# Optimization experiments

Measured on AMD Instinct MI355X. Metric: run time of the kernel, lower is better.

Reference implementation:

```python
import jax, jax.numpy as jnp
import numpy as np

HIDDEN = 1024
HEADS = 16
HEAD = HIDDEN // HEADS


def setup_inputs() -> dict:
    key = jax.random.key(0)
    ks = jax.random.split(key, 10)
    s = 1.0 / np.sqrt(HIDDEN)
    inp = {
        "x": jax.random.normal(ks[0], (2, 2048, HIDDEN), dtype=jnp.float32),
        "Wq": jax.random.uniform(ks[1], (HIDDEN, HIDDEN), jnp.float32, -s, s),
        "bq": jnp.zeros((HIDDEN,), jnp.float32),
        "Wk": jax.random.uniform(ks[2], (HIDDEN, HIDDEN), jnp.float32, -s, s),
        "bk": jnp.zeros((HIDDEN,), jnp.float32),
        "Wv": jax.random.uniform(ks[3], (HIDDEN, HIDDEN), jnp.float32, -s, s),
        "bv": jnp.zeros((HIDDEN,), jnp.float32),
        "Wo": jax.random.uniform(ks[4], (HIDDEN, HIDDEN), jnp.float32, -s, s),
        "bo": jnp.zeros((HIDDEN,), jnp.float32),
        "ln_g": jnp.ones((HIDDEN,), jnp.float32),
        "ln_b": jnp.zeros((HIDDEN,), jnp.float32),
    }
    return inp


def reference(x, Wq, bq, Wk, bk, Wv, bv, Wo, bo, ln_g, ln_b):
    B, S, H = x.shape
    # pre-LN (eps=1e-5 like torch LayerNorm)
    mu = jnp.mean(x, axis=-1, keepdims=True)
    var = jnp.mean(jnp.square(x - mu), axis=-1, keepdims=True)
    xn = (x - mu) * jax.lax.rsqrt(var + 1e-5) * ln_g + ln_b
    # QKV projections (torch Linear: x @ W.T + b) -> [B,S,heads,head]
    q = (xn @ Wq.T + bq).reshape(B, S, HEADS, HEAD)
    k = (xn @ Wk.T + bk).reshape(B, S, HEADS, HEAD)
    v = (xn @ Wv.T + bv).reshape(B, S, HEADS, HEAD)
    # scaled dot-product attention, naive full scores [B,heads,S,S]
    scores = jnp.einsum("bqhd,bkhd->bhqk", q, k) / jnp.sqrt(jnp.float32(HEAD))
    attn = jax.nn.softmax(scores, axis=-1)
    ctx = jnp.einsum("bhqk,bkhd->bqhd", attn, v).reshape(B, S, H)
    out = ctx @ Wo.T + bo
    return x + out  # dropout is identity in eval
```

## Files before the change

kernel.cpp:

```cpp
#include <hip/hip_runtime.h>
#include <hip/hip_bf16.h>
#include <stdint.h>

#define HID 1024
#define SEQ 2048
#define BATCH 2
#define NHEADS 16
#define HEADDIM 64
#define MROWS (BATCH*SEQ)

#define GAS __attribute__((address_space(1)))
#define LAS __attribute__((address_space(3)))

typedef __attribute__((ext_vector_type(8))) __bf16 bf16x8;
typedef __attribute__((ext_vector_type(4))) float f32x4;
typedef __attribute__((ext_vector_type(16))) float f32x16;

__device__ __forceinline__ ushort f2bf(float f) {
  union { float f; uint32_t u; } v; v.f = f;
  return (ushort)((v.u + 0x7FFFu + ((v.u >> 16) & 1u)) >> 16);
}

__device__ __forceinline__ void gl_lds16(const void* g, void* l) {
  __builtin_amdgcn_global_load_lds((const GAS void*)g, (LAS void*)l, 16, 0, 0);
}

__device__ __forceinline__ uint32_t cvtpk(float a, float b) {
  uint32_t r;
  asm("v_cvt_pk_bf16_f32 %0, %1, %2" : "=v"(r) : "v"(a), "v"(b));
  return r;
}

__device__ __forceinline__ void pl32swap(uint32_t& a, uint32_t& b) {
  asm("v_permlane32_swap_b32 %0, %1" : "+v"(a), "+v"(b));
}

__global__ __launch_bounds__(256) void k_cvt(const float* __restrict__ Wq,
                                             const float* __restrict__ Wk,
                                             const float* __restrict__ Wv,
                                             const float* __restrict__ Wo,
                                             ushort* __restrict__ dst) {
  int mat = blockIdx.y;
  const float* src = (mat == 0) ? Wq : (mat == 1) ? Wk : (mat == 2) ? Wv : Wo;
  int off = (blockIdx.x * 256 + threadIdx.x) * 4;
  float4 v = *(const float4*)(src + off);
  ushort4 o;
  o.x = f2bf(v.x); o.y = f2bf(v.y); o.z = f2bf(v.z); o.w = f2bf(v.w);
  *(ushort4*)(dst + (size_t)mat * (HID * HID) + off) = o;
}

__global__ __launch_bounds__(256) void k_ln(const float* __restrict__ x,
                                            const float* __restrict__ g,
                                            const float* __restrict__ b,
                                            ushort* __restrict__ xn) {
  int row = blockIdx.x;
  int t = threadIdx.x;
  const float* xr = x + (size_t)row * HID;
  float4 v = *(const float4*)(xr + t * 4);
  float s = v.x + v.y + v.z + v.w;
  float s2 = v.x * v.x + v.y * v.y + v.z * v.z + v.w * v.w;
  for (int m = 1; m < 64; m <<= 1) { s += __shfl_xor(s, m); s2 += __shfl_xor(s2, m); }
  __shared__ float ws[4], ws2[4];
  int wid = t >> 6;
  if ((t & 63) == 0) { ws[wid] = s; ws2[wid] = s2; }
  __syncthreads();
  s = ws[0] + ws[1] + ws[2] + ws[3];
  s2 = ws2[0] + ws2[1] + ws2[2] + ws2[3];
  float mu = s * (1.0f / HID);
  float var = s2 * (1.0f / HID) - mu * mu;
  float rstd = rsqrtf(var + 1e-5f);
  float4 gg = *(const float4*)(g + t * 4);
  float4 bb = *(const float4*)(b + t * 4);
  ushort4 o;
  o.x = f2bf((v.x - mu) * rstd * gg.x + bb.x);
  o.y = f2bf((v.y - mu) * rstd * gg.y + bb.y);
  o.z = f2bf((v.z - mu) * rstd * gg.z + bb.z);
  o.w = f2bf((v.w - mu) * rstd * gg.w + bb.w);
  *(ushort4*)(xn + (size_t)row * HID + t * 4) = o;
}

__global__ __launch_bounds__(256) void k_qkv(const ushort* __restrict__ xn,
                                             const ushort* __restrict__ wmat,
                                             const float* __restrict__ bq,
                                             const float* __restrict__ bk,
                                             const float* __restrict__ bv,
                                             ushort* __restrict__ qo,
                                             ushort* __restrict__ ko,
                                             ushort* __restrict__ vo) {
  __shared__ ushort As[128 * 32];
  __shared__ ushort Bs[128 * 32];
  int tid = threadIdx.x;
  int lane = tid & 63;
  int wv = tid >> 6;
  int quad = lane >> 4;
  int l16 = lane & 15;
  int m0 = blockIdx.x * 128;
  int ng = blockIdx.y * 128;
  int mat = ng >> 10;
  int nloc = ng & 1023;
  const ushort* wptr = wmat + (size_t)mat * (HID * HID) + (size_t)nloc * HID;
  const float* bias = (mat == 0) ? bq : (mat == 1) ? bk : bv;
  ushort* outp = (mat == 0) ? qo : (mat == 1) ? ko : vo;
  const float scl = (mat == 0) ? 0.18033688011112042f : 1.0f;

  int arow = tid >> 2;
  int acol = (tid & 3) * 8;
  int wm = (wv >> 1) * 64, wn = (wv & 1) * 64;

  f32x4 acc[4][4] = {};
  for (int k0 = 0; k0 < HID; k0 += 32) {
    __syncthreads();
    for (int t = 0; t < 2; t++) {
      gl_lds16(xn + (size_t)(m0 + t * 64 + arow) * HID + k0 + acol,
               As + t * 2048 + wv * 512);
      gl_lds16(wptr + (size_t)(t * 64 + arow) * HID + k0 + acol,
               Bs + t * 2048 + wv * 512);
    }
    __syncthreads();
    bf16x8 af[4], bfr[4];
    for (int i = 0; i < 4; i++)
      af[i] = *(const bf16x8*)&As[(wm + i * 16 + l16) * 32 + quad * 8];
    for (int n = 0; n < 4; n++)
      bfr[n] = *(const bf16x8*)&Bs[(wn + n * 16 + l16) * 32 + quad * 8];
    for (int i = 0; i < 4; i++)
      for (int n = 0; n < 4; n++)
        acc[i][n] = __builtin_amdgcn_mfma_f32_16x16x32_bf16(af[i], bfr[n], acc[i][n], 0, 0, 0);
  }
  float bv4[4];
  for (int n = 0; n < 4; n++) bv4[n] = bias[nloc + wn + n * 16 + l16];
  for (int i = 0; i < 4; i++) {
    int mrow = m0 + wm + i * 16 + quad * 4;
    for (int n = 0; n < 4; n++) {
      int col = nloc + wn + n * 16 + l16;
      int h = col >> 6, d = col & 63;
      for (int r = 0; r < 4; r++) {
        int m = mrow + r;
        int bidx = m >> 11, sidx = m & 2047;
        size_t dst;
        if (mat == 2)
          dst = (((size_t)(bidx * NHEADS + h) * HEADDIM) + d) * SEQ + sidx;
        else
          dst = (((size_t)(bidx * NHEADS + h) * SEQ) + sidx) * HEADDIM + d;
        outp[dst] = f2bf((acc[i][n][r] + bv4[n]) * scl);
      }
    }
  }
}

#define E2(x) __builtin_amdgcn_exp2f(fminf((x), 80.f))

#define SOFTMAX_PF(S0, S1)                                                     \
    union { uint32_t u[4]; bf16x8 v; } pf0, pf1, pf2, pf3;                     \
    {                                                                          \
      uint32_t c0 = cvtpk(E2(S0[0]),  E2(S0[1]));                              \
      uint32_t c1 = cvtpk(E2(S0[2]),  E2(S0[3]));                              \
      uint32_t c2 = cvtpk(E2(S0[4]),  E2(S0[5]));                              \
      uint32_t c3 = cvtpk(E2(S0[6]),  E2(S0[7]));                              \
      uint32_t c4 = cvtpk(E2(S0[8]),  E2(S0[9]));                              \
      uint32_t c5 = cvtpk(E2(S0[10]), E2(S0[11]));                             \
      uint32_t c6 = cvtpk(E2(S0[12]), E2(S0[13]));                             \
      uint32_t c7 = cvtpk(E2(S0[14]), E2(S0[15]));                             \
      pl32swap(c0, c2); pl32swap(c1, c3); pl32swap(c4, c6); pl32swap(c5, c7);  \
      pf0.u[0] = c0; pf0.u[1] = c1; pf0.u[2] = c2; pf0.u[3] = c3;              \
      pf1.u[0] = c4; pf1.u[1] = c5; pf1.u[2] = c6; pf1.u[3] = c7;              \
    }                                                                          \
    {                                                                          \
      uint32_t c0 = cvtpk(E2(S1[0]),  E2(S1[1]));                              \
      uint32_t c1 = cvtpk(E2(S1[2]),  E2(S1[3]));                              \
      uint32_t c2 = cvtpk(E2(S1[4]),  E2(S1[5]));                              \
      uint32_t c3 = cvtpk(E2(S1[6]),  E2(S1[7]));                              \
      uint32_t c4 = cvtpk(E2(S1[8]),  E2(S1[9]));                              \
      uint32_t c5 = cvtpk(E2(S1[10]), E2(S1[11]));                             \
      uint32_t c6 = cvtpk(E2(S1[12]), E2(S1[13]));                             \
      uint32_t c7 = cvtpk(E2(S1[14]), E2(S1[15]));                             \
      pl32swap(c0, c2); pl32swap(c1, c3); pl32swap(c4, c6); pl32swap(c5, c7);  \
      pf2.u[0] = c0; pf2.u[1] = c1; pf2.u[2] = c2; pf2.u[3] = c3;              \
      pf3.u[0] = c4; pf3.u[1] = c5; pf3.u[2] = c6; pf3.u[3] = c7;              \
    }

#define ATTN_BODY(T, SC0, SC1, SP0, SP1, DO_DMA)                               \
  do {                                                                         \
    if (DO_DMA) {                                                              \
      size_t ko = (size_t)((T) + 1) * 64 * HEADDIM;                            \
      size_t vo = (size_t)((T) + 1) * 64;                                      \
      int kn = kc ^ 1;                                                         \
      gl_lds16(kSrcA + ko, &Ksm[kn][ldsA]);                                    \
      gl_lds16(kSrcB + ko, &Ksm[kn][ldsB]);                                    \
      gl_lds16(vSrcA + vo, &Vsm[vn][ldsA]);                                    \
      gl_lds16(vSrcB + vo, &Vsm[vn][ldsB]);                                    \
    }                                                                          \
    SC0 = (f32x16){}; SC1 = (f32x16){};                                        \
    __builtin_amdgcn_s_setprio(1);                                             \
    _Pragma("unroll")                                                          \
    for (int f = 0; f < 4; f++) {                                              \
      int g = 2 * f + hi;                                                      \
      bf16x8 k0 = *(const bf16x8*)&Ksm[kc][l32 * 64 + ((g ^ rsw) * 8)];        \
      bf16x8 k1 = *(const bf16x8*)&Ksm[kc][(32 + l32) * 64 + ((g ^ rsw) * 8)]; \
      SC0 = __builtin_amdgcn_mfma_f32_32x32x16_bf16(k0, qf[f], SC0, 0, 0, 0);  \
      SC1 = __builtin_amdgcn_mfma_f32_32x32x16_bf16(k1, qf[f], SC1, 0, 0, 0);  \
    }                                                                          \
    __builtin_amdgcn_s_setprio(0);                                             \
    bf16x8 vf[8];                                                              \
    _Pragma("unroll")                                                          \
    for (int kf = 0; kf < 4; kf++) {                                           \
      int g = 2 * kf + hi;                                                     \
      vf[2 * kf]     = *(const bf16x8*)&Vsm[vp][l32 * 64 + ((g ^ rsw) * 8)];   \
      vf[2 * kf + 1] = *(const bf16x8*)&Vsm[vp][(32 + l32) * 64 + ((g ^ rsw) * 8)]; \
    }                                                                          \
    SOFTMAX_PF(SP0, SP1)                                                       \
    __builtin_amdgcn_s_setprio(1);                                             \
    _Pragma("unroll")                                                          \
    for (int kf = 0; kf < 4; kf++) {                                           \
      bf16x8 pv = (kf == 0) ? pf0.v : (kf == 1) ? pf1.v : (kf == 2) ? pf2.v : pf3.v; \
      Oa0 = __builtin_amdgcn_mfma_f32_32x32x16_bf16(pv, vf[2 * kf], Oa0, 0, 0, 0);   \
      Oa1 = __builtin_amdgcn_mfma_f32_32x32x16_bf16(pv, vf[2 * kf + 1], Oa1, 0, 0, 0); \
      Os  = __builtin_amdgcn_mfma_f32_32x32x16_bf16(pv, ones, Os, 0, 0, 0);    \
    }                                                                          \
    __builtin_amdgcn_s_setprio(0);                                             \
    __syncthreads();                                                           \
    if (DO_DMA) kc ^= 1;                                                       \
    { int tmp = vp; vp = vc; vc = vn; vn = tmp; }                              \
  } while (0)

__global__ __launch_bounds__(256, 2) void k_attn(const ushort* __restrict__ Q,
                                                 const ushort* __restrict__ K,
                                                 const ushort* __restrict__ Vt,
                                                 ushort* __restrict__ ctx) {
  __shared__ ushort Ksm[2][64 * 64];
  __shared__ ushort Vsm[3][64 * 64];
  int tid = threadIdx.x, lane = tid & 63, wv = tid >> 6;
  int l32 = lane & 31, hi = lane >> 5;
  int bh = blockIdx.x;
  int q0 = blockIdx.y * 128;
  const ushort* Qb = Q + ((size_t)bh * SEQ + q0 + wv * 32 + l32) * HEADDIM;
  const ushort* Kb = K + (size_t)bh * SEQ * HEADDIM;
  const ushort* Vb = Vt + (size_t)bh * HEADDIM * SEQ;

  bf16x8 qf[4];
#pragma unroll
  for (int f = 0; f < 4; f++)
    qf[f] = *(const bf16x8*)(Qb + f * 16 + hi * 8);

  bf16x8 ones;
#pragma unroll
  for (int j = 0; j < 8; j++) ones[j] = (__bf16)1.0f;

  int gsl = lane & 7;
  int rowA = wv * 8 + (lane >> 3);
  int rowB = 32 + wv * 8 + (lane >> 3);
  const ushort* kSrcA = Kb + rowA * HEADDIM + ((gsl ^ (rowA & 7)) * 8);
  const ushort* kSrcB = Kb + rowB * HEADDIM + ((gsl ^ (rowB & 7)) * 8);
  const ushort* vSrcA = Vb + (size_t)rowA * SEQ + ((gsl ^ (rowA & 7)) * 8);
  const ushort* vSrcB = Vb + (size_t)rowB * SEQ + ((gsl ^ (rowB & 7)) * 8);
  int ldsA = wv * 512;
  int ldsB = 2048 + wv * 512;

  f32x16 Oa0 = {}, Oa1 = {}, Os = {};
  f32x16 sA0, sA1, sB0, sB1;
  int rsw = (l32 & 7);

  gl_lds16(kSrcA, &Ksm[0][ldsA]);
  gl_lds16(kSrcB, &Ksm[0][ldsB]);
  gl_lds16(vSrcA, &Vsm[0][ldsA]);
  gl_lds16(vSrcB, &Vsm[0][ldsB]);
  __syncthreads();

  {
    size_t ko = (size_t)64 * HEADDIM;
    size_t vo = (size_t)64;
    gl_lds16(kSrcA + ko, &Ksm[1][ldsA]);
    gl_lds16(kSrcB + ko, &Ksm[1][ldsB]);
    gl_lds16(vSrcA + vo, &Vsm[1][ldsA]);
    gl_lds16(vSrcB + vo, &Vsm[1][ldsB]);
    sA0 = (f32x16){}; sA1 = (f32x16){};
    __builtin_amdgcn_s_setprio(1);
#pragma unroll
    for (int f = 0; f < 4; f++) {
      int g = 2 * f + hi;
      bf16x8 k0 = *(const bf16x8*)&Ksm[0][l32 * 64 + ((g ^ rsw) * 8)];
      bf16x8 k1 = *(const bf16x8*)&Ksm[0][(32 + l32) * 64 + ((g ^ rsw) * 8)];
      sA0 = __builtin_amdgcn_mfma_f32_32x32x16_bf16(k0, qf[f], sA0, 0, 0, 0);
      sA1 = __builtin_amdgcn_mfma_f32_32x32x16_bf16(k1, qf[f], sA1, 0, 0, 0);
    }
    __builtin_amdgcn_s_setprio(0);
    __syncthreads();
  }

  int kc = 1, vp = 0, vc = 1, vn = 2;
  for (int t = 1; t < 31; t += 2) {
    ATTN_BODY(t,     sB0, sB1, sA0, sA1, true);
    ATTN_BODY(t + 1, sA0, sA1, sB0, sB1, true);
  }
  ATTN_BODY(31, sB0, sB1, sA0, sA1, false);

  {
    bf16x8 vf[8];
#pragma unroll
    for (int kf = 0; kf < 4; kf++) {
      int g = 2 * kf + hi;
      vf[2 * kf]     = *(const bf16x8*)&Vsm[vp][l32 * 64 + ((g ^ rsw) * 8)];
      vf[2 * kf + 1] = *(const bf16x8*)&Vsm[vp][(32 + l32) * 64 + ((g ^ rsw) * 8)];
    }
    SOFTMAX_PF(sB0, sB1)
    __builtin_amdgcn_s_setprio(1);
#pragma unroll
    for (int kf = 0; kf < 4; kf++) {
      bf16x8 pv = (kf == 0) ? pf0.v : (kf == 1) ? pf1.v : (kf == 2) ? pf2.v : pf3.v;
      Oa0 = __builtin_amdgcn_mfma_f32_32x32x16_bf16(pv, vf[2 * kf], Oa0, 0, 0, 0);
      Oa1 = __builtin_amdgcn_mfma_f32_32x32x16_bf16(pv, vf[2 * kf + 1], Oa1, 0, 0, 0);
      Os  = __builtin_amdgcn_mfma_f32_32x32x16_bf16(pv, ones, Os, 0, 0, 0);
    }
    __builtin_amdgcn_s_setprio(0);
  }

  int bidx = bh >> 4, h = bh & 15;
#pragma unroll
  for (int r = 0; r < 16; r++) {
    float inv = 1.0f / Os[r];
    int qloc = (r & 3) + 8 * (r >> 2) + 4 * hi;
    int sidx = q0 + wv * 32 + qloc;
    size_t base = ((size_t)(bidx * SEQ) + sidx) * HID + h * HEADDIM;
    ctx[base + l32]      = f2bf(Oa0[r] * inv);
    ctx[base + 32 + l32] = f2bf(Oa1[r] * inv);
  }
}

__global__ __launch_bounds__(256) void k_oproj(const ushort* __restrict__ ctx,
                                               const ushort* __restrict__ wmat,
                                               const float* __restrict__ bo,
                                               const float* __restrict__ x,
                                               float* __restrict__ out) {
  __shared__ ushort As[128 * 32];
  __shared__ ushort Bs[128 * 32];
  int tid = threadIdx.x;
  int lane = tid & 63;
  int wv = tid >> 6;
  int quad = lane >> 4;
  int l16 = lane & 15;
  int m0 = blockIdx.x * 128;
  int n0 = blockIdx.y * 128;
  const ushort* wptr = wmat + (size_t)3 * (HID * HID) + (size_t)n0 * HID;
  int arow = tid >> 2;
  int acol = (tid & 3) * 8;
  int wm = (wv >> 1) * 64, wn = (wv & 1) * 64;

  f32x4 acc[4][4] = {};
  for (int k0 = 0; k0 < HID; k0 += 32) {
    __syncthreads();
    for (int t = 0; t < 2; t++) {
      gl_lds16(ctx + (size_t)(m0 + t * 64 + arow) * HID + k0 + acol,
               As + t * 2048 + wv * 512);
      gl_lds16(wptr + (size_t)(t * 64 + arow) * HID + k0 + acol,
               Bs + t * 2048 + wv * 512);
    }
    __syncthreads();
    bf16x8 af[4], bfr[4];
    for (int i = 0; i < 4; i++)
      af[i] = *(const bf16x8*)&As[(wm + i * 16 + l16) * 32 + quad * 8];
    for (int n = 0; n < 4; n++)
      bfr[n] = *(const bf16x8*)&Bs[(wn + n * 16 + l16) * 32 + quad * 8];
    for (int i = 0; i < 4; i++)
      for (int n = 0; n < 4; n++)
        acc[i][n] = __builtin_amdgcn_mfma_f32_16x16x32_bf16(af[i], bfr[n], acc[i][n], 0, 0, 0);
  }
  float bv4[4];
  for (int n = 0; n < 4; n++) bv4[n] = bo[n0 + wn + n * 16 + l16];
  for (int i = 0; i < 4; i++) {
    int mrow = m0 + wm + i * 16 + quad * 4;
    for (int n = 0; n < 4; n++) {
      int col = n0 + wn + n * 16 + l16;
      for (int r = 0; r < 4; r++) {
        size_t idx = (size_t)(mrow + r) * HID + col;
        out[idx] = acc[i][n][r] + bv4[n] + x[idx];
      }
    }
  }
}

extern "C" void kernel_launch(void* const* d_in, const int* in_sizes, int n_in,
                              void* d_out, int out_size, void* d_ws, size_t ws_size,
                              hipStream_t stream) {
  const float* x    = (const float*)d_in[0];
  const float* Wq   = (const float*)d_in[1];
  const float* bq   = (const float*)d_in[2];
  const float* Wk   = (const float*)d_in[3];
  const float* bk   = (const float*)d_in[4];
  const float* Wv   = (const float*)d_in[5];
  const float* bv   = (const float*)d_in[6];
  const float* Wo   = (const float*)d_in[7];
  const float* bo   = (const float*)d_in[8];
  const float* ln_g = (const float*)d_in[9];
  const float* ln_b = (const float*)d_in[10];
  float* out = (float*)d_out;

  const size_t MB = 1024 * 1024;
  ushort* ws_w = (ushort*)d_ws;
  ushort* xn   = (ushort*)((char*)d_ws + 8 * MB);
  ushort* Qw   = (ushort*)((char*)d_ws + 16 * MB);
  ushort* Kw   = (ushort*)((char*)d_ws + 24 * MB);
  ushort* Vw   = (ushort*)((char*)d_ws + 32 * MB);
  ushort* Cw   = (ushort*)((char*)d_ws + 40 * MB);

  k_cvt<<<dim3(1024, 4), 256, 0, stream>>>(Wq, Wk, Wv, Wo, ws_w);
  k_ln<<<dim3(MROWS), 256, 0, stream>>>(x, ln_g, ln_b, xn);
  k_qkv<<<dim3(32, 24), 256, 0, stream>>>(xn, ws_w, bq, bk, bv, Qw, Kw, Vw);
  k_attn<<<dim3(BATCH * NHEADS, SEQ / 128), 256, 0, stream>>>(Qw, Kw, Vw, Cw);
  k_oproj<<<dim3(32, 8), 256, 0, stream>>>(Cw, ws_w, bo, x, out);
}
```

Baseline: 206.7 us.

## Deepen attention K/V prefetch to two tiles ahead with counted vmcnt waits

Grows the K ring to three buffers and the V ring to four, and issues each tile's global-to-LDS loads two tiles ahead instead of one. The full __syncthreads drain is replaced by s_waitcnt vmcnt(4) plus a raw barrier, so the most recent prefetch can stay in flight across the barrier. The exp2 input clamp is also dropped to save a VALU op per score. The trade is more LDS per block, which could limit occupancy, and the loss of overflow protection if scores are ever large.

New measurement: 200.4 us. -3.1%, faster.

```diff
diff --git a/kernel.cpp b/kernel.cpp
--- a/kernel.cpp
+++ b/kernel.cpp
@@ -147,7 +147,7 @@
   }
 }
 
-#define E2(x) __builtin_amdgcn_exp2f(fminf((x), 80.f))
+#define E2(x) __builtin_amdgcn_exp2f(x)
 
 #define SOFTMAX_PF(S0, S1)                                                     \
     union { uint32_t u[4]; bf16x8 v; } pf0, pf1, pf2, pf3;                     \
@@ -178,24 +178,23 @@
       pf3.u[0] = c4; pf3.u[1] = c5; pf3.u[2] = c6; pf3.u[3] = c7;              \
     }
 
-#define ATTN_BODY(T, SC0, SC1, SP0, SP1, DO_DMA)                               \
+#define ATTN_BODY(T, SC0, SC1, SP0, SP1, DO_DMA, WAITN)                        \
   do {                                                                         \
     if (DO_DMA) {                                                              \
-      size_t ko = (size_t)((T) + 1) * 64 * HEADDIM;                            \
-      size_t vo = (size_t)((T) + 1) * 64;                                      \
-      int kn = kc ^ 1;                                                         \
-      gl_lds16(kSrcA + ko, &Ksm[kn][ldsA]);                                    \
-      gl_lds16(kSrcB + ko, &Ksm[kn][ldsB]);                                    \
-      gl_lds16(vSrcA + vo, &Vsm[vn][ldsA]);                                    \
-      gl_lds16(vSrcB + vo, &Vsm[vn][ldsB]);                                    \
+      size_t ko = (size_t)((T) + 2) * 64 * HEADDIM;                            \
+      size_t vo = (size_t)((T) + 2) * 64;                                      \
+      gl_lds16(kSrcA + ko, &Ksm[kd][ldsA]);                                    \
+      gl_lds16(kSrcB + ko, &Ksm[kd][ldsB]);                                    \
+      gl_lds16(vSrcA + vo, &Vsm[vd][ldsA]);                                    \
+      gl_lds16(vSrcB + vo, &Vsm[vd][ldsB]);                                    \
     }                                                                          \
     SC0 = (f32x16){}; SC1 = (f32x16){};                                        \
     __builtin_amdgcn_s_setprio(1);                                             \
     _Pragma("unroll")                                                          \
     for (int f = 0; f < 4; f++) {                                              \
       int g = 2 * f + hi;                                                      \
-      bf16x8 k0 = *(const bf16x8*)&Ksm[kc][l32 * 64 + ((g ^ rsw) * 8)];        \
-      bf16x8 k1 = *(const bf16x8*)&Ksm[kc][(32 + l32) * 64 + ((g ^ rsw) * 8)]; \
+      bf16x8 k0 = *(const bf16x8*)&Ksm[kr][l32 * 64 + ((g ^ rsw) * 8)];        \
+      bf16x8 k1 = *(const bf16x8*)&Ksm[kr][(32 + l32) * 64 + ((g ^ rsw) * 8)]; \
       SC0 = __builtin_amdgcn_mfma_f32_32x32x16_bf16(k0, qf[f], SC0, 0, 0, 0);  \
       SC1 = __builtin_amdgcn_mfma_f32_32x32x16_bf16(k1, qf[f], SC1, 0, 0, 0);  \
     }                                                                          \
@@ -204,8 +203,8 @@
     _Pragma("unroll")                                                          \
     for (int kf = 0; kf < 4; kf++) {                                           \
       int g = 2 * kf + hi;                                                     \
-      vf[2 * kf]     = *(const bf16x8*)&Vsm[vp][l32 * 64 + ((g ^ rsw) * 8)];   \
-      vf[2 * kf + 1] = *(const bf16x8*)&Vsm[vp][(32 + l32) * 64 + ((g ^ rsw) * 8)]; \
+      vf[2 * kf]     = *(const bf16x8*)&Vsm[vr][l32 * 64 + ((g ^ rsw) * 8)];   \
+      vf[2 * kf + 1] = *(const bf16x8*)&Vsm[vr][(32 + l32) * 64 + ((g ^ rsw) * 8)]; \
     }                                                                          \
     SOFTMAX_PF(SP0, SP1)                                                       \
     __builtin_amdgcn_s_setprio(1);                                             \
@@ -217,17 +216,21 @@
       Os  = __builtin_amdgcn_mfma_f32_32x32x16_bf16(pv, ones, Os, 0, 0, 0);    \
     }                                                                          \
     __builtin_amdgcn_s_setprio(0);                                             \
-    __syncthreads();                                                           \
-    if (DO_DMA) kc ^= 1;                                                       \
-    { int tmp = vp; vp = vc; vc = vn; vn = tmp; }                              \
+    asm volatile("s_waitcnt vmcnt(" #WAITN ")" ::: "memory");                  \
+    __builtin_amdgcn_s_barrier();                                              \
+    __builtin_amdgcn_sched_barrier(0);                                         \
+    kr = (kr == 2) ? 0 : kr + 1;                                               \
+    kd = (kd == 2) ? 0 : kd + 1;                                               \
+    vr = (vr + 1) & 3;                                                         \
+    vd = (vd + 1) & 3;                                                         \
   } while (0)
 
 __global__ __launch_bounds__(256, 2) void k_attn(const ushort* __restrict__ Q,
                                                  const ushort* __restrict__ K,
                                                  const ushort* __restrict__ Vt,
                                                  ushort* __restrict__ ctx) {
-  __shared__ ushort Ksm[2][64 * 64];
-  __shared__ ushort Vsm[3][64 * 64];
+  __shared__ ushort Ksm[3][64 * 64];
+  __shared__ ushort Vsm[4][64 * 64];
   int tid = threadIdx.x, lane = tid & 63, wv = tid >> 6;
   int l32 = lane & 31, hi = lane >> 5;
   int bh = blockIdx.x;
@@ -263,15 +266,19 @@
   gl_lds16(kSrcB, &Ksm[0][ldsB]);
   gl_lds16(vSrcA, &Vsm[0][ldsA]);
   gl_lds16(vSrcB, &Vsm[0][ldsB]);
-  __syncthreads();
+  gl_lds16(kSrcA + 64 * HEADDIM, &Ksm[1][ldsA]);
+  gl_lds16(kSrcB + 64 * HEADDIM, &Ksm[1][ldsB]);
+  gl_lds16(vSrcA + 64, &Vsm[1][ldsA]);
+  gl_lds16(vSrcB + 64, &Vsm[1][ldsB]);
+  asm volatile("s_waitcnt vmcnt(4)" ::: "memory");
+  __builtin_amdgcn_s_barrier();
+  __builtin_amdgcn_sched_barrier(0);
 
   {
-    size_t ko = (size_t)64 * HEADDIM;
-    size_t vo = (size_t)64;
-    gl_lds16(kSrcA + ko, &Ksm[1][ldsA]);
-    gl_lds16(kSrcB + ko, &Ksm[1][ldsB]);
-    gl_lds16(vSrcA + vo, &Vsm[1][ldsA]);
-    gl_lds16(vSrcB + vo, &Vsm[1][ldsB]);
+    gl_lds16(kSrcA + 2 * 64 * HEADDIM, &Ksm[2][ldsA]);
+    gl_lds16(kSrcB + 2 * 64 * HEADDIM, &Ksm[2][ldsB]);
+    gl_lds16(vSrcA + 2 * 64, &Vsm[2][ldsA]);
+    gl_lds16(vSrcB + 2 * 64, &Vsm[2][ldsB]);
     sA0 = (f32x16){}; sA1 = (f32x16){};
     __builtin_amdgcn_s_setprio(1);
 #pragma unroll
@@ -283,23 +290,58 @@
       sA1 = __builtin_amdgcn_mfma_f32_32x32x16_bf16(k1, qf[f], sA1, 0, 0, 0);
     }
     __builtin_amdgcn_s_setprio(0);
-    __syncthreads();
-  }
-
-  int kc = 1, vp = 0, vc = 1, vn = 2;
-  for (int t = 1; t < 31; t += 2) {
-    ATTN_BODY(t,     sB0, sB1, sA0, sA1, true);
-    ATTN_BODY(t + 1, sA0, sA1, sB0, sB1, true);
-  }
-  ATTN_BODY(31, sB0, sB1, sA0, sA1, false);
+    asm volatile("s_waitcnt vmcnt(4)" ::: "memory");
+    __builtin_amdgcn_s_barrier();
+    __builtin_amdgcn_sched_barrier(0);
+  }
+
+  int kr = 1, kd = 0, vr = 0, vd = 3;
+  for (int t = 1; t < 29; t += 2) {
+    ATTN_BODY(t,     sB0, sB1, sA0, sA1, true, 4);
+    ATTN_BODY(t + 1, sA0, sA1, sB0, sB1, true, 4);
+  }
+  ATTN_BODY(29, sB0, sB1, sA0, sA1, true, 4);
+  ATTN_BODY(30, sA0, sA1, sB0, sB1, false, 0);
+
+  {
+    sB0 = (f32x16){}; sB1 = (f32x16){};
+    __builtin_amdgcn_s_setprio(1);
+#pragma unroll
+    for (int f = 0; f < 4; f++) {
+      int g = 2 * f + hi;
+      bf16x8 k0 = *(const bf16x8*)&Ksm[kr][l32 * 64 + ((g ^ rsw) * 8)];
+      bf16x8 k1 = *(const bf16x8*)&Ksm[kr][(32 + l32) * 64 + ((g ^ rsw) * 8)];
+      sB0 = __builtin_amdgcn_mfma_f32_32x32x16_bf16(k0, qf[f], sB0, 0, 0, 0);
+      sB1 = __builtin_amdgcn_mfma_f32_32x32x16_bf16(k1, qf[f], sB1, 0, 0, 0);
+    }
+    __builtin_amdgcn_s_setprio(0);
+    bf16x8 vf[8];
+#pragma unroll
+    for (int kf = 0; kf < 4; kf++) {
+      int g = 2 * kf + hi;
+      vf[2 * kf]     = *(const bf16x8*)&Vsm[vr][l32 * 64 + ((g ^ rsw) * 8)];
+      vf[2 * kf + 1] = *(const bf16x8*)&Vsm[vr][(32 + l32) * 64 + ((g ^ rsw) * 8)];
+    }
+    SOFTMAX_PF(sA0, sA1)
+    __builtin_amdgcn_s_setprio(1);
+#pragma unroll
+    for (int kf = 0; kf < 4; kf++) {
+      bf16x8 pv = (kf == 0) ? pf0.v : (kf == 1) ? pf1.v : (kf == 2) ? pf2.v : pf3.v;
+      Oa0 = __builtin_amdgcn_mfma_f32_32x32x16_bf16(pv, vf[2 * kf], Oa0, 0, 0, 0);
+      Oa1 = __builtin_amdgcn_mfma_f32_32x32x16_bf16(pv, vf[2 * kf + 1], Oa1, 0, 0, 0);
+      Os  = __builtin_amdgcn_mfma_f32_32x32x16_bf16(pv, ones, Os, 0, 0, 0);
+    }
+    __builtin_amdgcn_s_setprio(0);
+    vr = (vr + 1) & 3;
+  }
 
   {
     bf16x8 vf[8];
 #pragma unroll
     for (int kf = 0; kf < 4; kf++) {
       int g = 2 * kf + hi;
-      vf[2 * kf]     = *(const bf16x8*)&Vsm[vp][l32 * 64 + ((g ^ rsw) * 8)];
-      vf[2 * kf + 1] = *(const bf16x8*)&Vsm[vp][(32 + l32) * 64 + ((g ^ rsw) * 8)];
+      vf[2 * kf]     = *(const bf16x8*)&Vsm[vr][l32 * 64 + ((g ^ rsw) * 8)];
+      vf[2 * kf + 1] = *(const bf16x8*)&Vsm[vr][(32 + l32) * 64 + ((g ^ rsw) * 8)];
     }
     SOFTMAX_PF(sB0, sB1)
     __builtin_amdgcn_s_setprio(1);
```
